# Optimization experiments

Hardware: AMD Instinct MI355X
Metric: run time of the kernel (lower is better)

## Reference

```python
import jax, jax.numpy as jnp
import numpy as np

N = 2048       # num nodes
E = 4096       # num edges
D_NODE = 128
D_EDGE = 128
H = 4          # heads
DH = D_EDGE // H
C = 16         # num classes
NODE_K = N // 2   # node_k_ratio = 0.5
EDGE_K = E // 2   # edge_k_ratio = 0.5
NEG = -1e9


def setup_inputs() -> dict:
    key = jax.random.key(0)
    ks = jax.random.split(key, 16)
    w = lambda k, shape: jax.random.normal(k, shape, jnp.float32) * 0.02
    return {
        "node_features": jax.random.normal(ks[0], (N, D_NODE), jnp.float32),
        "edge_features": jax.random.normal(ks[1], (E, D_EDGE), jnp.float32),
        "edge_index": jax.random.randint(ks[2], (2, E), 0, N, jnp.int32),
        # ImportanceRouter: scalar scores per node / edge
        "w_router_n": w(ks[3], (D_NODE,)),
        "w_router_e": w(ks[4], (D_EDGE,)),
        # EdgeAttention projections
        "w_e": w(ks[5], (D_EDGE, D_EDGE)),
        "w_n": w(ks[6], (D_NODE, D_EDGE)),
        "w_q": w(ks[7], (D_EDGE, D_EDGE)),
        "w_k": w(ks[8], (D_EDGE, D_EDGE)),
        "w_v": w(ks[9], (D_EDGE, D_EDGE)),
        "w_o": w(ks[10], (D_EDGE, D_EDGE)),
        # classifier MLP: Linear -> GELU -> Linear
        "w1": w(ks[11], (D_EDGE, D_EDGE)),
        "b1": jnp.zeros((D_EDGE,), jnp.float32),
        "w2": w(ks[12], (D_EDGE, C)),
        "b2": jnp.zeros((C,), jnp.float32),
    }


def reference(node_features, edge_features, edge_index,
              w_router_n, w_router_e,
              w_e, w_n, w_q, w_k, w_v, w_o,
              w1, b1, w2, b2):
    src, dst = edge_index[0], edge_index[1]

    # --- ImportanceRouter: node/edge scores ---
    ns = node_features @ w_router_n   # [N]
    es = edge_features @ w_router_e   # [E]

    # --- apply_top_k(node_k_ratio=0.5, edge_k_ratio=0.5) ---
    _, nidx = jax.lax.top_k(ns, NODE_K)
    node_mask = jnp.zeros((N,), bool).at[nidx].set(True)
    _, eidx = jax.lax.top_k(es, EDGE_K)
    edge_topk = jnp.zeros((E,), bool).at[eidx].set(True)
    edge_mask = edge_topk & node_mask[src] & node_mask[dst]   # [E]

    ef = edge_features * edge_mask[:, None].astype(edge_features.dtype)

    # --- build_edge_adjacency: edges sharing a node attend to each other ---
    adj = ((src[:, None] == src[None, :]) | (src[:, None] == dst[None, :]) |
           (dst[:, None] == src[None, :]) | (dst[:, None] == dst[None, :]))  # [E,E]

    # --- EdgeAttention: edge rep mixes edge feats and endpoint node feats ---
    h = ef @ w_e + (node_features[src] + node_features[dst]) @ w_n   # [E, D_EDGE]
    q = (h @ w_q).reshape(E, H, DH)
    k = (h @ w_k).reshape(E, H, DH)
    v = (h @ w_v).reshape(E, H, DH)
    scores = jnp.einsum('ehd,fhd->hef', q, k) / np.float32(np.sqrt(DH))  # [H,E,E]
    scores = jnp.where(adj[None, :, :], scores, NEG)
    attn = jax.nn.softmax(scores, axis=-1)
    o = jnp.einsum('hef,fhd->ehd', attn, v).reshape(E, D_EDGE) @ w_o    # [E, D_EDGE]

    # --- classifier: Linear -> GELU -> Linear ---
    x = jax.nn.gelu(o @ w1 + b1)
    logits = x @ w2 + b2            # [E, C]
    return logits
```

## Files before the change

kernel.cpp:

```cpp
#include <hip/hip_runtime.h>
#include <hip/hip_bf16.h>
#include <math.h>

#define NN 2048
#define NE 4096
#define D 128
#define NODE_K 1024
#define EDGE_K 2048
#define CAP 64

typedef const __hip_bfloat16* bfp;
typedef unsigned short u16;
typedef __attribute__((ext_vector_type(8))) short short8;
typedef __attribute__((ext_vector_type(4))) float floatx4;

#define MFMA16(a, b, c) __builtin_amdgcn_mfma_f32_16x16x32_bf16(a, b, c, 0, 0, 0)

__device__ __forceinline__ float b2f(__hip_bfloat16 x) { return __bfloat162float(x); }

__device__ __forceinline__ float ldx(const void* p, size_t i, int f) {
  return f ? ((const float*)p)[i] : b2f(((bfp)p)[i]);
}
__device__ __forceinline__ float4 ldx4(const void* p, size_t i4, int f) {
  if (f) return ((const float4*)p)[i4];
  ushort4 u = ((const ushort4*)p)[i4];
  float4 r;
  r.x = __uint_as_float(((unsigned)u.x) << 16);
  r.y = __uint_as_float(((unsigned)u.y) << 16);
  r.z = __uint_as_float(((unsigned)u.z) << 16);
  r.w = __uint_as_float(((unsigned)u.w) << 16);
  return r;
}

__device__ __forceinline__ void split2(float x, u16& hi, u16& lo) {
  unsigned u = __float_as_uint(x);
  unsigned h = (u + 0x7FFFu + ((u >> 16) & 1u)) >> 16;
  hi = (u16)h;
  float r = x - __uint_as_float(h << 16);
  unsigned v = __float_as_uint(r);
  lo = (u16)((v + 0x7FFFu + ((v >> 16) & 1u)) >> 16);
}
__device__ __forceinline__ void build_frags(const float* v8, short8& fh, short8& fl) {
  #pragma unroll
  for (int i = 0; i < 8; ++i) {
    u16 h, l;
    split2(v8[i], h, l);
    fh[i] = (short)h; fl[i] = (short)l;
  }
}

__device__ __forceinline__ int detect_f(const u16* raw, int* s4) {
  int t = threadIdx.x;
  int weird = 0;
  for (int i = t; i < 1024; i += blockDim.x) {
    unsigned int bits = ((unsigned int)raw[i]) << 16;
    float x = __uint_as_float(bits);
    float ax = fabsf(x);
    if (!(ax <= 1e3f) || (x != 0.f && ax < 1e-12f)) weird++;
  }
  #pragma unroll
  for (int m = 32; m >= 1; m >>= 1) weird += __shfl_xor(weird, m);
  int nw = (int)blockDim.x >> 6;
  if ((t & 63) == 0) s4[t >> 6] = weird;
  __syncthreads();
  int tot = 0;
  for (int i = 0; i < nw; ++i) tot += s4[i];
  return (tot > 50) ? 1 : 0;
}

struct K1Args {
  const void *nf, *ef, *wrn, *wre;
  const void* w[7];
  float *ns, *es;
  int *deg, *flag;
  u16 *wtHi, *wtLo;
  u16 *feHi, *feLo;
};

#define SCORE_BLOCKS ((NN + NE) / 4)
#define WPREP_BLOCKS 112
#define FSPLIT_BLOCKS 192
__global__ __launch_bounds__(256) void scores_prep_kernel(K1Args a) {
  __shared__ int s4[4];
  int b = blockIdx.x, t = threadIdx.x;
  int f = detect_f((const u16*)a.nf, s4);
  if (b < SCORE_BLOCKS) {
    int wid = b * 4 + (t >> 6), lane = t & 63;
    const void* base; const void* w; float* out; size_t r0;
    if (wid < NN) { base = a.nf; r0 = (size_t)wid * D; w = a.wrn; out = a.ns + wid; }
    else { int r = wid - NN; base = a.ef; r0 = (size_t)r * D; w = a.wre; out = a.es + r; }
    double p = (double)ldx(base, r0 + lane, f) * (double)ldx(w, lane, f)
             + (double)ldx(base, r0 + lane + 64, f) * (double)ldx(w, lane + 64, f);
    #pragma unroll
    for (int m = 32; m >= 1; m >>= 1) p += __shfl_xor(p, m);
    if (lane == 0) *out = (float)p;
  } else if (b == SCORE_BLOCKS) {
    if (t == 0) a.flag[0] = f;
    for (int i = t; i < NN; i += 256) a.deg[i] = 0;
  } else if (b <= SCORE_BLOCKS + WPREP_BLOCKS) {
    int tau = (b - SCORE_BLOCKS - 1) * 256 + t;
    int w = tau >> 12, rem = tau & 4095;
    int n = rem >> 5, k0 = (rem & 31) * 4;
    ushort4 hi, lo;
    split2(ldx(a.w[w], (size_t)(k0 + 0) * 128 + n, f), hi.x, lo.x);
    split2(ldx(a.w[w], (size_t)(k0 + 1) * 128 + n, f), hi.y, lo.y);
    split2(ldx(a.w[w], (size_t)(k0 + 2) * 128 + n, f), hi.z, lo.z);
    split2(ldx(a.w[w], (size_t)(k0 + 3) * 128 + n, f), hi.w, lo.w);
    ((ushort4*)a.wtHi)[tau] = hi;
    ((ushort4*)a.wtLo)[tau] = lo;
  } else {
    int fb = b - SCORE_BLOCKS - 1 - WPREP_BLOCKS;
    #pragma unroll
    for (int i = 0; i < 4; ++i) {
      int g4 = fb * 1024 + i * 256 + t;
      float4 x = (g4 < NN * D / 4) ? ldx4(a.nf, g4, f)
                                   : ldx4(a.ef, g4 - NN * D / 4, f);
      ushort4 hi, lo;
      split2(x.x, hi.x, lo.x);
      split2(x.y, hi.y, lo.y);
      split2(x.z, hi.z, lo.z);
      split2(x.w, hi.w, lo.w);
      ((ushort4*)a.feHi)[g4] = hi;
      ((ushort4*)a.feLo)[g4] = lo;
    }
  }
}

#define NMB (NN / 4)
#define EMB (NE / 4)
__global__ __launch_bounds__(256) void mask_lists_kernel(
    const float* __restrict__ ns, const float* __restrict__ es,
    const int* __restrict__ src, const int* __restrict__ dst,
    int* __restrict__ node_mask, int* __restrict__ edge_topk,
    int* __restrict__ deg, int* __restrict__ lists) {
  __shared__ __align__(16) float s[NE];
  int b = blockIdx.x, t = threadIdx.x;
  if (b < NMB) {
    for (int i = t; i < NN / 4; i += 256) ((float4*)s)[i] = ((const float4*)ns)[i];
    __syncthreads();
    int i = b * 4 + (t >> 6), lane = t & 63;
    float si = s[i];
    int rank = 0;
    for (int j = lane; j < NN; j += 64) {
      float sj = s[j];
      rank += (sj > si) || (sj == si && j < i);
    }
    #pragma unroll
    for (int m = 32; m >= 1; m >>= 1) rank += __shfl_xor(rank, m);
    if (lane == 0) node_mask[i] = (rank < NODE_K) ? 1 : 0;
  } else if (b < NMB + EMB) {
    for (int i = t; i < NE / 4; i += 256) ((float4*)s)[i] = ((const float4*)es)[i];
    __syncthreads();
    int i = (b - NMB) * 4 + (t >> 6), lane = t & 63;
    float si = s[i];
    int rank = 0;
    for (int j = lane; j < NE; j += 64) {
      float sj = s[j];
      rank += (sj > si) || (sj == si && j < i);
    }
    #pragma unroll
    for (int m = 32; m >= 1; m >>= 1) rank += __shfl_xor(rank, m);
    if (lane == 0) edge_topk[i] = (rank < EDGE_K) ? 1 : 0;
  } else {
    int e = (b - NMB - EMB) * 256 + t;
    if (e < NE) {
      int sn = src[e], dn = dst[e];
      int p = atomicAdd(&deg[sn], 1);
      if (p >= 0 && p < CAP) lists[sn * CAP + p] = e;
      if (dn != sn) {
        p = atomicAdd(&deg[dn], 1);
        if (p >= 0 && p < CAP) lists[dn * CAP + p] = e;
      }
    }
  }
}

__global__ __launch_bounds__(512) void h_qkv_mfma_kernel(
    const u16* __restrict__ feHi, const u16* __restrict__ feLo,
    const int* __restrict__ src, const int* __restrict__ dst,
    const int* __restrict__ node_mask, const int* __restrict__ edge_topk,
    const u16* __restrict__ wtHi, const u16* __restrict__ wtLo,
    float* __restrict__ qkv) {
  __shared__ __align__(16) float hf[8 * 64 * 4];
  int t = threadIdx.x;
  int wave = t >> 6, lane = t & 63;
  int qd = lane >> 4, c = lane & 15;
  int row0 = blockIdx.x * 16;
  int e = row0 + c;
  int sn = src[e], dn = dst[e];
  bool em = edge_topk[e] && node_mask[sn] && node_mask[dn];
  int n0 = wave * 16;
  const u16* efH = feHi + (size_t)NN * D;
  const u16* efL = feLo + (size_t)NN * D;
  const short8 z8 = {0, 0, 0, 0, 0, 0, 0, 0};

  short8 A1h[4], A1l[4], Sh[4], Sl[4], Dh[4], Dl[4];
  short8 BEh[4], BEl[4], BNh[4], BNl[4];
  #pragma unroll
  for (int ks = 0; ks < 4; ++ks) {
    int k0 = ks * 32 + qd * 8;
    A1h[ks] = *(const short8*)(efH + (size_t)e * D + k0);
    A1l[ks] = *(const short8*)(efL + (size_t)e * D + k0);
    Sh[ks]  = *(const short8*)(feHi + (size_t)sn * D + k0);
    Sl[ks]  = *(const short8*)(feLo + (size_t)sn * D + k0);
    Dh[ks]  = *(const short8*)(feHi + (size_t)dn * D + k0);
    Dl[ks]  = *(const short8*)(feLo + (size_t)dn * D + k0);
    size_t bo = (size_t)(n0 + c) * 128 + k0;
    BEh[ks] = *(const short8*)(wtHi + bo);
    BEl[ks] = *(const short8*)(wtLo + bo);
    BNh[ks] = *(const short8*)(wtHi + 16384 + bo);
    BNl[ks] = *(const short8*)(wtLo + 16384 + bo);
  }
  if (!em) {
    #pragma unroll
    for (int ks = 0; ks < 4; ++ks) { A1h[ks] = z8; A1l[ks] = z8; }
  }
  floatx4 accE = {0.f, 0.f, 0.f, 0.f};
  floatx4 accN = {0.f, 0.f, 0.f, 0.f};
  #pragma unroll
  for (int ks = 0; ks < 4; ++ks) {
    accE = MFMA16(A1h[ks], BEh[ks], accE);
    accN = MFMA16(Sh[ks], BNh[ks], accN);
    accE = MFMA16(A1l[ks], BEh[ks], accE);
    accN = MFMA16(Sl[ks], BNh[ks], accN);
    accE = MFMA16(A1h[ks], BEl[ks], accE);
    accN = MFMA16(Sh[ks], BNl[ks], accN);
    accN = MFMA16(Dh[ks], BNh[ks], accN);
    accN = MFMA16(Dl[ks], BNh[ks], accN);
    accN = MFMA16(Dh[ks], BNl[ks], accN);
  }
  {
    int np = n0 + c;
    int kd = np >> 5, qq = (np >> 3) & 3, half = (c >> 2) & 1, j4 = c & 3;
    #pragma unroll
    for (int r = 0; r < 4; ++r)
      hf[((kd * 2 + half) * 64 + qq * 16 + 4 * qd + r) * 4 + j4] = accE[r] + accN[r];
  }
  short8 BQh[4], BQl[4], BKh[4], BKl[4], BVh[4], BVl[4];
  #pragma unroll
  for (int ks = 0; ks < 4; ++ks) {
    size_t bo = (size_t)(n0 + c) * 128 + ks * 32 + qd * 8;
    BQh[ks] = *(const short8*)(wtHi + 2 * 16384 + bo);
    BQl[ks] = *(const short8*)(wtLo + 2 * 16384 + bo);
    BKh[ks] = *(const short8*)(wtHi + 3 * 16384 + bo);
    BKl[ks] = *(const short8*)(wtLo + 3 * 16384 + bo);
    BVh[ks] = *(const short8*)(wtHi + 4 * 16384 + bo);
    BVl[ks] = *(const short8*)(wtLo + 4 * 16384 + bo);
  }
  __syncthreads();
  floatx4 aq = {0.f, 0.f, 0.f, 0.f};
  floatx4 ak = {0.f, 0.f, 0.f, 0.f};
  floatx4 av = {0.f, 0.f, 0.f, 0.f};
  #pragma unroll
  for (int ks = 0; ks < 4; ++ks) {
    float4 p0 = *(const float4*)&hf[((ks * 2 + 0) * 64 + lane) * 4];
    float4 p1 = *(const float4*)&hf[((ks * 2 + 1) * 64 + lane) * 4];
    float v8[8] = {p0.x, p0.y, p0.z, p0.w, p1.x, p1.y, p1.z, p1.w};
    short8 ah, al;
    build_frags(v8, ah, al);
    aq = MFMA16(ah, BQh[ks], aq);
    ak = MFMA16(ah, BKh[ks], ak);
    av = MFMA16(ah, BVh[ks], av);
    aq = MFMA16(al, BQh[ks], aq);
    ak = MFMA16(al, BKh[ks], ak);
    av = MFMA16(al, BVh[ks], av);
    aq = MFMA16(ah, BQl[ks], aq);
    ak = MFMA16(ah, BKl[ks], ak);
    av = MFMA16(ah, BVl[ks], av);
  }
  #pragma unroll
  for (int r = 0; r < 4; ++r) {
    size_t ro = (size_t)(row0 + 4 * qd + r) * D + n0 + c;
    qkv[ro] = aq[r];
    qkv[(size_t)NE * D + ro] = ak[r];
    qkv[(size_t)2 * NE * D + ro] = av[r];
  }
}

__global__ void attn_kernel(const float* __restrict__ q, const float* __restrict__ k,
                            const float* __restrict__ v, const int* __restrict__ src,
                            const int* __restrict__ dst, const int* __restrict__ deg,
                            const int* __restrict__ lists, float* __restrict__ ao) {
  int e = blockIdx.x;
  int j = threadIdx.x;
  float qj = q[(size_t)e * D + j];
  int sn = src[e], dn = dst[e];
  float m = -1e30f, l = 0.f, acc = 0.f;
  const float scale = 0.17677669529663687f;
  int degA = max(0, min(deg[sn], CAP));
  for (int i = 0; i < degA; ++i) {
    int fe = lists[sn * CAP + i];
    float p = qj * k[(size_t)fe * D + j];
    p += __shfl_xor(p, 16); p += __shfl_xor(p, 8); p += __shfl_xor(p, 4);
    p += __shfl_xor(p, 2);  p += __shfl_xor(p, 1);
    float s = p * scale;
    float vj = v[(size_t)fe * D + j];
    float mn = fmaxf(m, s);
    float corr = expf(m - mn);
    float w = expf(s - mn);
    l = l * corr + w;
    acc = acc * corr + w * vj;
    m = mn;
  }
  if (dn != sn) {
    int degB = max(0, min(deg[dn], CAP));
    for (int i = 0; i < degB; ++i) {
      int fe = lists[dn * CAP + i];
      if (src[fe] == sn || dst[fe] == sn) continue;
      float p = qj * k[(size_t)fe * D + j];
      p += __shfl_xor(p, 16); p += __shfl_xor(p, 8); p += __shfl_xor(p, 4);
      p += __shfl_xor(p, 2);  p += __shfl_xor(p, 1);
      float s = p * scale;
      float vj = v[(size_t)fe * D + j];
      float mn = fmaxf(m, s);
      float corr = expf(m - mn);
      float w = expf(s - mn);
      l = l * corr + w;
      acc = acc * corr + w * vj;
      m = mn;
    }
  }
  ao[(size_t)e * D + j] = acc / fmaxf(l, 1e-37f);
}

__global__ __launch_bounds__(512) void o_mlp_mfma_kernel(
    const float* __restrict__ ao,
    const u16* __restrict__ wtHi, const u16* __restrict__ wtLo,
    const void* __restrict__ b1, const void* __restrict__ w2,
    const void* __restrict__ b2, const int* __restrict__ flag,
    void* __restrict__ out) {
  __shared__ __align__(16) float hf[8 * 64 * 4];
  __shared__ float xl[16 * 132];
  __shared__ float w2l[128 * 16];
  int t = threadIdx.x;
  int wave = t >> 6, lane = t & 63;
  int qd = lane >> 4, c = lane & 15;
  int f = flag[0];
  int row0 = blockIdx.x * 16;
  int n0 = wave * 16;

  short8 BOh[4], BOl[4], B1h[4], B1l[4];
  #pragma unroll
  for (int ks = 0; ks < 4; ++ks) {
    size_t bo = (size_t)(n0 + c) * 128 + ks * 32 + qd * 8;
    BOh[ks] = *(const short8*)(wtHi + 5 * 16384 + bo);
    BOl[ks] = *(const short8*)(wtLo + 5 * 16384 + bo);
    B1h[ks] = *(const short8*)(wtHi + 6 * 16384 + bo);
    B1l[ks] = *(const short8*)(wtLo + 6 * 16384 + bo);
  }
  floatx4 acc = {0.f, 0.f, 0.f, 0.f};
  #pragma unroll
  for (int ks = 0; ks < 4; ++ks) {
    int k0 = ks * 32 + qd * 8;
    const float* ap = ao + (size_t)(row0 + c) * D + k0;
    float4 p0 = *(const float4*)ap;
    float4 p1 = *(const float4*)(ap + 4);
    float v8[8] = {p0.x, p0.y, p0.z, p0.w, p1.x, p1.y, p1.z, p1.w};
    short8 ah, al;
    build_frags(v8, ah, al);
    acc = MFMA16(ah, BOh[ks], acc);
    acc = MFMA16(al, BOh[ks], acc);
    acc = MFMA16(ah, BOl[ks], acc);
  }
  {
    int np = n0 + c;
    int kd = np >> 5, qq = (np >> 3) & 3, half = (c >> 2) & 1, j4 = c & 3;
    #pragma unroll
    for (int r = 0; r < 4; ++r)
      hf[((kd * 2 + half) * 64 + qq * 16 + 4 * qd + r) * 4 + j4] = acc[r];
  }
  __syncthreads();
  floatx4 a2c = {0.f, 0.f, 0.f, 0.f};
  #pragma unroll
  for (int ks = 0; ks < 4; ++ks) {
    float4 p0 = *(const float4*)&hf[((ks * 2 + 0) * 64 + lane) * 4];
    float4 p1 = *(const float4*)&hf[((ks * 2 + 1) * 64 + lane) * 4];
    float v8[8] = {p0.x, p0.y, p0.z, p0.w, p1.x, p1.y, p1.z, p1.w};
    short8 ah, al;
    build_frags(v8, ah, al);
    a2c = MFMA16(ah, B1h[ks], a2c);
    a2c = MFMA16(al, B1h[ks], a2c);
    a2c = MFMA16(ah, B1l[ks], a2c);
  }
  float bj = ldx(b1, n0 + c, f);
  #pragma unroll
  for (int r = 0; r < 4; ++r) {
    float u = a2c[r] + bj;
    float inner = 0.7978845608028654f * (u + 0.044715f * u * u * u);
    xl[(4 * qd + r) * 132 + n0 + c] = 0.5f * u * (1.f + tanhf(inner));
  }
  for (int i = t; i < D * 16; i += 512) w2l[i] = ldx(w2, i, f);
  __syncthreads();
  if (t < 256) {
    int r = t >> 4, cc = t & 15;
    float s = 0.f;
    for (int kk = 0; kk < D; ++kk) s += xl[r * 132 + kk] * w2l[kk * 16 + cc];
    s += ldx(b2, cc, f);
    int idx = (row0 + r) * 16 + cc;
    if (f) ((float*)out)[idx] = s;
    else ((__hip_bfloat16*)out)[idx] = __float2bfloat16(s);
  }
}

extern "C" void kernel_launch(void* const* d_in, const int* in_sizes, int n_in,
                              void* d_out, int out_size, void* d_ws, size_t ws_size,
                              hipStream_t stream) {
  const int* eidx = (const int*)d_in[2];
  const int* src = eidx;
  const int* dst = eidx + NE;

  size_t off = 0;
  char* base = (char*)d_ws;
  auto alloc = [&](size_t nbytes) -> void* {
    void* p = base + off;
    off += (nbytes + 255) & ~(size_t)255;
    return p;
  };
  int* flag      = (int*)alloc(256);
  float* ns      = (float*)alloc(NN * sizeof(float));
  float* es      = (float*)alloc(NE * sizeof(float));
  int* node_mask = (int*)alloc(NN * sizeof(int));
  int* edge_topk = (int*)alloc(NE * sizeof(int));
  int* deg       = (int*)alloc(NN * sizeof(int));
  int* lists     = (int*)alloc((size_t)NN * CAP * sizeof(int));
  u16* wtHi      = (u16*)alloc((size_t)7 * 16384 * sizeof(u16));
  u16* wtLo      = (u16*)alloc((size_t)7 * 16384 * sizeof(u16));
  u16* feHi      = (u16*)alloc((size_t)(NN + NE) * D * sizeof(u16));
  u16* feLo      = (u16*)alloc((size_t)(NN + NE) * D * sizeof(u16));
  float* qkv     = (float*)alloc((size_t)3 * NE * D * sizeof(float));
  float* ao      = (float*)alloc((size_t)NE * D * sizeof(float));
  float* qb = qkv, *kb = qkv + NE * D, *vb = qkv + 2 * NE * D;

  K1Args a1;
  a1.nf = d_in[0]; a1.ef = d_in[1]; a1.wrn = d_in[3]; a1.wre = d_in[4];
  a1.w[0] = d_in[5];  a1.w[1] = d_in[6];  a1.w[2] = d_in[7];
  a1.w[3] = d_in[8];  a1.w[4] = d_in[9];  a1.w[5] = d_in[10]; a1.w[6] = d_in[11];
  a1.ns = ns; a1.es = es; a1.deg = deg; a1.flag = flag;
  a1.wtHi = wtHi; a1.wtLo = wtLo; a1.feHi = feHi; a1.feLo = feLo;

  scores_prep_kernel<<<SCORE_BLOCKS + 1 + WPREP_BLOCKS + FSPLIT_BLOCKS, 256, 0,
                       stream>>>(a1);
  mask_lists_kernel<<<NMB + EMB + NE / 256, 256, 0, stream>>>(
      ns, es, src, dst, node_mask, edge_topk, deg, lists);
  h_qkv_mfma_kernel<<<NE / 16, 512, 0, stream>>>(
      feHi, feLo, src, dst, node_mask, edge_topk, wtHi, wtLo, qkv);
  attn_kernel<<<NE, 128, 0, stream>>>(qb, kb, vb, src, dst, deg, lists, ao);
  o_mlp_mfma_kernel<<<NE / 16, 512, 0, stream>>>(
      ao, wtHi, wtLo, d_in[12], d_in[13], d_in[14], flag, d_out);
}
```

Baseline: 139.2 us.

## Split attention neighbor loop across four thread groups and vectorize top-k and MLP loops

The attention kernel now runs 512 threads per edge, with four groups each handling every fourth neighbor. The partial online-softmax states (max, sum, accumulator) are merged through shared memory at the end, which shortens the serial neighbor chain per edge. The top-k ranking reads scores directly from global memory as float4 instead of first staging them in shared memory, and the final 128x16 classifier stage stores w2 transposed so its dot product can use float4 reads. The split attention adds a block barrier and extra exp calls for the merge, and most groups sit idle when node degree is small.

```diff
diff --git a/kernel.cpp b/kernel.cpp
--- a/kernel.cpp
+++ b/kernel.cpp
@@ -133,30 +133,33 @@
     const int* __restrict__ src, const int* __restrict__ dst,
     int* __restrict__ node_mask, int* __restrict__ edge_topk,
     int* __restrict__ deg, int* __restrict__ lists) {
-  __shared__ __align__(16) float s[NE];
   int b = blockIdx.x, t = threadIdx.x;
   if (b < NMB) {
-    for (int i = t; i < NN / 4; i += 256) ((float4*)s)[i] = ((const float4*)ns)[i];
-    __syncthreads();
     int i = b * 4 + (t >> 6), lane = t & 63;
-    float si = s[i];
+    float si = ns[i];
     int rank = 0;
-    for (int j = lane; j < NN; j += 64) {
-      float sj = s[j];
-      rank += (sj > si) || (sj == si && j < i);
+    for (int j4 = lane; j4 < NN / 4; j4 += 64) {
+      float4 sj = ((const float4*)ns)[j4];
+      int j = j4 * 4;
+      rank += (sj.x > si) || (sj.x == si && j + 0 < i);
+      rank += (sj.y > si) || (sj.y == si && j + 1 < i);
+      rank += (sj.z > si) || (sj.z == si && j + 2 < i);
+      rank += (sj.w > si) || (sj.w == si && j + 3 < i);
     }
     #pragma unroll
     for (int m = 32; m >= 1; m >>= 1) rank += __shfl_xor(rank, m);
     if (lane == 0) node_mask[i] = (rank < NODE_K) ? 1 : 0;
   } else if (b < NMB + EMB) {
-    for (int i = t; i < NE / 4; i += 256) ((float4*)s)[i] = ((const float4*)es)[i];
-    __syncthreads();
     int i = (b - NMB) * 4 + (t >> 6), lane = t & 63;
-    float si = s[i];
+    float si = es[i];
     int rank = 0;
-    for (int j = lane; j < NE; j += 64) {
-      float sj = s[j];
-      rank += (sj > si) || (sj == si && j < i);
+    for (int j4 = lane; j4 < NE / 4; j4 += 64) {
+      float4 sj = ((const float4*)es)[j4];
+      int j = j4 * 4;
+      rank += (sj.x > si) || (sj.x == si && j + 0 < i);
+      rank += (sj.y > si) || (sj.y == si && j + 1 < i);
+      rank += (sj.z > si) || (sj.z == si && j + 2 < i);
+      rank += (sj.w > si) || (sj.w == si && j + 3 < i);
     }
     #pragma unroll
     for (int m = 32; m >= 1; m >>= 1) rank += __shfl_xor(rank, m);
@@ -277,24 +280,27 @@
   }
 }
 
-__global__ void attn_kernel(const float* __restrict__ q, const float* __restrict__ k,
-                            const float* __restrict__ v, const int* __restrict__ src,
-                            const int* __restrict__ dst, const int* __restrict__ deg,
-                            const int* __restrict__ lists, float* __restrict__ ao) {
+__global__ __launch_bounds__(512) void attn_kernel(
+    const float* __restrict__ q, const float* __restrict__ k,
+    const float* __restrict__ v, const int* __restrict__ src,
+    const int* __restrict__ dst, const int* __restrict__ deg,
+    const int* __restrict__ lists, float* __restrict__ ao) {
+  __shared__ float sm[4][128], sl[4][128], sa[4][128];
   int e = blockIdx.x;
-  int j = threadIdx.x;
-  float qj = q[(size_t)e * D + j];
+  int t = threadIdx.x;
+  int par = t >> 7, jj = t & 127;
+  float qj = q[(size_t)e * D + jj];
   int sn = src[e], dn = dst[e];
   float m = -1e30f, l = 0.f, acc = 0.f;
   const float scale = 0.17677669529663687f;
   int degA = max(0, min(deg[sn], CAP));
-  for (int i = 0; i < degA; ++i) {
+  for (int i = par; i < degA; i += 4) {
     int fe = lists[sn * CAP + i];
-    float p = qj * k[(size_t)fe * D + j];
+    float p = qj * k[(size_t)fe * D + jj];
     p += __shfl_xor(p, 16); p += __shfl_xor(p, 8); p += __shfl_xor(p, 4);
     p += __shfl_xor(p, 2);  p += __shfl_xor(p, 1);
     float s = p * scale;
-    float vj = v[(size_t)fe * D + j];
+    float vj = v[(size_t)fe * D + jj];
     float mn = fmaxf(m, s);
     float corr = expf(m - mn);
     float w = expf(s - mn);
@@ -304,14 +310,14 @@
   }
   if (dn != sn) {
     int degB = max(0, min(deg[dn], CAP));
-    for (int i = 0; i < degB; ++i) {
+    for (int i = par; i < degB; i += 4) {
       int fe = lists[dn * CAP + i];
       if (src[fe] == sn || dst[fe] == sn) continue;
-      float p = qj * k[(size_t)fe * D + j];
+      float p = qj * k[(size_t)fe * D + jj];
       p += __shfl_xor(p, 16); p += __shfl_xor(p, 8); p += __shfl_xor(p, 4);
       p += __shfl_xor(p, 2);  p += __shfl_xor(p, 1);
       float s = p * scale;
-      float vj = v[(size_t)fe * D + j];
+      float vj = v[(size_t)fe * D + jj];
       float mn = fmaxf(m, s);
       float corr = expf(m - mn);
       float w = expf(s - mn);
@@ -320,7 +326,22 @@
       m = mn;
     }
   }
-  ao[(size_t)e * D + j] = acc / fmaxf(l, 1e-37f);
+  sm[par][jj] = m; sl[par][jj] = l; sa[par][jj] = acc;
+  __syncthreads();
+  if (par == 0) {
+    float M = m;
+    #pragma unroll
+    for (int p2 = 1; p2 < 4; ++p2) M = fmaxf(M, sm[p2][jj]);
+    float cs = expf(m - M);
+    float L = l * cs, A = acc * cs;
+    #pragma unroll
+    for (int p2 = 1; p2 < 4; ++p2) {
+      float c2 = expf(sm[p2][jj] - M);
+      L += sl[p2][jj] * c2;
+      A += sa[p2][jj] * c2;
+    }
+    ao[(size_t)e * D + jj] = A / fmaxf(L, 1e-37f);
+  }
 }
 
 __global__ __launch_bounds__(512) void o_mlp_mfma_kernel(
@@ -330,8 +351,8 @@
     const void* __restrict__ b2, const int* __restrict__ flag,
     void* __restrict__ out) {
   __shared__ __align__(16) float hf[8 * 64 * 4];
-  __shared__ float xl[16 * 132];
-  __shared__ float w2l[128 * 16];
+  __shared__ __align__(16) float xl[16 * 132];
+  __shared__ __align__(16) float w2t[16 * 132];
   int t = threadIdx.x;
   int wave = t >> 6, lane = t & 63;
   int qd = lane >> 4, c = lane & 15;
@@ -389,12 +410,21 @@
     float inner = 0.7978845608028654f * (u + 0.044715f * u * u * u);
     xl[(4 * qd + r) * 132 + n0 + c] = 0.5f * u * (1.f + tanhf(inner));
   }
-  for (int i = t; i < D * 16; i += 512) w2l[i] = ldx(w2, i, f);
+  for (int i = t; i < D * 16; i += 512) {
+    int kk = i >> 4, cc = i & 15;
+    w2t[cc * 132 + kk] = ldx(w2, i, f);
+  }
   __syncthreads();
   if (t < 256) {
     int r = t >> 4, cc = t & 15;
+    const float4* xr = (const float4*)&xl[r * 132];
+    const float4* wr = (const float4*)&w2t[cc * 132];
     float s = 0.f;
-    for (int kk = 0; kk < D; ++kk) s += xl[r * 132 + kk] * w2l[kk * 16 + cc];
+    #pragma unroll
+    for (int k4 = 0; k4 < D / 4; ++k4) {
+      float4 xa = xr[k4], wb = wr[k4];
+      s += xa.x * wb.x + xa.y * wb.y + xa.z * wb.z + xa.w * wb.w;
+    }
     s += ldx(b2, cc, f);
     int idx = (row0 + r) * 16 + cc;
     if (f) ((float*)out)[idx] = s;
@@ -444,7 +474,7 @@
       ns, es, src, dst, node_mask, edge_topk, deg, lists);
   h_qkv_mfma_kernel<<<NE / 16, 512, 0, stream>>>(
       feHi, feLo, src, dst, node_mask, edge_topk, wtHi, wtLo, qkv);
-  attn_kernel<<<NE, 128, 0, stream>>>(qb, kb, vb, src, dst, deg, lists, ao);
+  attn_kernel<<<NE, 512, 0, stream>>>(qb, kb, vb, src, dst, deg, lists, ao);
   o_mlp_mfma_kernel<<<NE / 16, 512, 0, stream>>>(
       ao, wtHi, wtLo, d_in[12], d_in[13], d_in[14], flag, d_out);
 }
```

After: 144.9 us. 1.04x slower.

## Fuse top-k masking into QKV kernel and attention into MLP kernel

Applied to the files above, without the earlier changes.

Five launches become three. The adjacency-list build moves into the prep kernel as a single block using LDS atomics. The top-k rank computation moves into the QKV kernel, computed only for the edges and endpoints each block needs. Attention is fused with the output projection and MLP in a 1024-thread block, so the attention output stays in LDS, and the w2 dot product is vectorised through a transposed LDS copy. This removes launch overhead and the global round trip for ao and the masks. The cost is a serial one-block list build, recomputation of node ranks per edge, and __syncthreads calls placed inside divergent branches, which is fragile.

```diff
diff --git a/kernel.cpp b/kernel.cpp
--- a/kernel.cpp
+++ b/kernel.cpp
@@ -49,10 +49,11 @@
   }
 }
 
-__device__ __forceinline__ int detect_f(const u16* raw, int* s4) {
+template <int NT>
+__device__ __forceinline__ int detect_f(const u16* raw, int* s8) {
   int t = threadIdx.x;
   int weird = 0;
-  for (int i = t; i < 1024; i += blockDim.x) {
+  for (int i = t; i < 1024; i += NT) {
     unsigned int bits = ((unsigned int)raw[i]) << 16;
     float x = __uint_as_float(bits);
     float ax = fabsf(x);
@@ -60,19 +61,20 @@
   }
   #pragma unroll
   for (int m = 32; m >= 1; m >>= 1) weird += __shfl_xor(weird, m);
-  int nw = (int)blockDim.x >> 6;
-  if ((t & 63) == 0) s4[t >> 6] = weird;
+  if ((t & 63) == 0) s8[t >> 6] = weird;
   __syncthreads();
   int tot = 0;
-  for (int i = 0; i < nw; ++i) tot += s4[i];
+  #pragma unroll
+  for (int i = 0; i < NT / 64; ++i) tot += s8[i];
   return (tot > 50) ? 1 : 0;
 }
 
 struct K1Args {
   const void *nf, *ef, *wrn, *wre;
   const void* w[7];
+  const int *src, *dst;
   float *ns, *es;
-  int *deg, *flag;
+  int *deg, *lists, *flag;
   u16 *wtHi, *wtLo;
   u16 *feHi, *feLo;
 };
@@ -80,10 +82,11 @@
 #define SCORE_BLOCKS ((NN + NE) / 4)
 #define WPREP_BLOCKS 112
 #define FSPLIT_BLOCKS 192
-__global__ __launch_bounds__(256) void scores_prep_kernel(K1Args a) {
-  __shared__ int s4[4];
+#define K1_BLOCKS (SCORE_BLOCKS + WPREP_BLOCKS + FSPLIT_BLOCKS + 1)
+__global__ __launch_bounds__(256) void scores_prep_lists_kernel(K1Args a) {
+  __shared__ int s8[4];
   int b = blockIdx.x, t = threadIdx.x;
-  int f = detect_f((const u16*)a.nf, s4);
+  int f = detect_f<256>((const u16*)a.nf, s8);
   if (b < SCORE_BLOCKS) {
     int wid = b * 4 + (t >> 6), lane = t & 63;
     const void* base; const void* w; float* out; size_t r0;
@@ -94,11 +97,8 @@
     #pragma unroll
     for (int m = 32; m >= 1; m >>= 1) p += __shfl_xor(p, m);
     if (lane == 0) *out = (float)p;
-  } else if (b == SCORE_BLOCKS) {
-    if (t == 0) a.flag[0] = f;
-    for (int i = t; i < NN; i += 256) a.deg[i] = 0;
-  } else if (b <= SCORE_BLOCKS + WPREP_BLOCKS) {
-    int tau = (b - SCORE_BLOCKS - 1) * 256 + t;
+  } else if (b < SCORE_BLOCKS + WPREP_BLOCKS) {
+    int tau = (b - SCORE_BLOCKS) * 256 + t;
     int w = tau >> 12, rem = tau & 4095;
     int n = rem >> 5, k0 = (rem & 31) * 4;
     ushort4 hi, lo;
@@ -108,8 +108,8 @@
     split2(ldx(a.w[w], (size_t)(k0 + 3) * 128 + n, f), hi.w, lo.w);
     ((ushort4*)a.wtHi)[tau] = hi;
     ((ushort4*)a.wtLo)[tau] = lo;
-  } else {
-    int fb = b - SCORE_BLOCKS - 1 - WPREP_BLOCKS;
+  } else if (b < SCORE_BLOCKS + WPREP_BLOCKS + FSPLIT_BLOCKS) {
+    int fb = b - SCORE_BLOCKS - WPREP_BLOCKS;
     #pragma unroll
     for (int i = 0; i < 4; ++i) {
       int g4 = fb * 1024 + i * 256 + t;
@@ -123,72 +123,65 @@
       ((ushort4*)a.feHi)[g4] = hi;
       ((ushort4*)a.feLo)[g4] = lo;
     }
-  }
-}
-
-#define NMB (NN / 4)
-#define EMB (NE / 4)
-__global__ __launch_bounds__(256) void mask_lists_kernel(
+  } else {
+    __shared__ int ldeg[NN];
+    for (int i = t; i < NN; i += 256) ldeg[i] = 0;
+    __syncthreads();
+    #pragma unroll
+    for (int i = 0; i < NE / 256; ++i) {
+      int e = i * 256 + t;
+      int sn = a.src[e], dn = a.dst[e];
+      int p = atomicAdd(&ldeg[sn], 1);
+      if (p < CAP) a.lists[sn * CAP + p] = e;
+      if (dn != sn) {
+        p = atomicAdd(&ldeg[dn], 1);
+        if (p < CAP) a.lists[dn * CAP + p] = e;
+      }
+    }
+    __syncthreads();
+    for (int i = t; i < NN; i += 256) a.deg[i] = ldeg[i];
+    if (t == 0) a.flag[0] = f;
+  }
+}
+
+__global__ __launch_bounds__(512) void h_qkv_mfma_kernel(
     const float* __restrict__ ns, const float* __restrict__ es,
-    const int* __restrict__ src, const int* __restrict__ dst,
-    int* __restrict__ node_mask, int* __restrict__ edge_topk,
-    int* __restrict__ deg, int* __restrict__ lists) {
-  __shared__ __align__(16) float s[NE];
-  int b = blockIdx.x, t = threadIdx.x;
-  if (b < NMB) {
-    for (int i = t; i < NN / 4; i += 256) ((float4*)s)[i] = ((const float4*)ns)[i];
-    __syncthreads();
-    int i = b * 4 + (t >> 6), lane = t & 63;
-    float si = s[i];
-    int rank = 0;
-    for (int j = lane; j < NN; j += 64) {
-      float sj = s[j];
-      rank += (sj > si) || (sj == si && j < i);
-    }
-    #pragma unroll
-    for (int m = 32; m >= 1; m >>= 1) rank += __shfl_xor(rank, m);
-    if (lane == 0) node_mask[i] = (rank < NODE_K) ? 1 : 0;
-  } else if (b < NMB + EMB) {
-    for (int i = t; i < NE / 4; i += 256) ((float4*)s)[i] = ((const float4*)es)[i];
-    __syncthreads();
-    int i = (b - NMB) * 4 + (t >> 6), lane = t & 63;
-    float si = s[i];
-    int rank = 0;
-    for (int j = lane; j < NE; j += 64) {
-      float sj = s[j];
-      rank += (sj > si) || (sj == si && j < i);
-    }
-    #pragma unroll
-    for (int m = 32; m >= 1; m >>= 1) rank += __shfl_xor(rank, m);
-    if (lane == 0) edge_topk[i] = (rank < EDGE_K) ? 1 : 0;
-  } else {
-    int e = (b - NMB - EMB) * 256 + t;
-    if (e < NE) {
-      int sn = src[e], dn = dst[e];
-      int p = atomicAdd(&deg[sn], 1);
-      if (p >= 0 && p < CAP) lists[sn * CAP + p] = e;
-      if (dn != sn) {
-        p = atomicAdd(&deg[dn], 1);
-        if (p >= 0 && p < CAP) lists[dn * CAP + p] = e;
-      }
-    }
-  }
-}
-
-__global__ __launch_bounds__(512) void h_qkv_mfma_kernel(
     const u16* __restrict__ feHi, const u16* __restrict__ feLo,
     const int* __restrict__ src, const int* __restrict__ dst,
-    const int* __restrict__ node_mask, const int* __restrict__ edge_topk,
     const u16* __restrict__ wtHi, const u16* __restrict__ wtLo,
     float* __restrict__ qkv) {
   __shared__ __align__(16) float hf[8 * 64 * 4];
+  __shared__ int s_msk[3][16];
   int t = threadIdx.x;
   int wave = t >> 6, lane = t & 63;
   int qd = lane >> 4, c = lane & 15;
   int row0 = blockIdx.x * 16;
+
+  for (int task = wave; task < 48; task += 8) {
+    int kind = task >> 4, ti = task & 15;
+    int e2 = row0 + ti;
+    const float* arr; int len, K, tgt;
+    if (kind == 0) { arr = es; len = NE; K = EDGE_K; tgt = e2; }
+    else { arr = ns; len = NN; K = NODE_K; tgt = (kind == 1) ? src[e2] : dst[e2]; }
+    float si = arr[tgt];
+    int rank = 0;
+    for (int j4 = lane; j4 < (len >> 2); j4 += 64) {
+      float4 sj = ((const float4*)arr)[j4];
+      int j = j4 * 4;
+      rank += (sj.x > si) || (sj.x == si && j + 0 < tgt);
+      rank += (sj.y > si) || (sj.y == si && j + 1 < tgt);
+      rank += (sj.z > si) || (sj.z == si && j + 2 < tgt);
+      rank += (sj.w > si) || (sj.w == si && j + 3 < tgt);
+    }
+    #pragma unroll
+    for (int m = 32; m >= 1; m >>= 1) rank += __shfl_xor(rank, m);
+    if (lane == 0) s_msk[kind][ti] = (rank < K) ? 1 : 0;
+  }
+  __syncthreads();
+
   int e = row0 + c;
   int sn = src[e], dn = dst[e];
-  bool em = edge_topk[e] && node_mask[sn] && node_mask[dn];
+  bool em = s_msk[0][c] && s_msk[1][c] && s_msk[2][c];
   int n0 = wave * 16;
   const u16* efH = feHi + (size_t)NN * D;
   const u16* efL = feLo + (size_t)NN * D;
@@ -277,124 +270,151 @@
   }
 }
 
-__global__ void attn_kernel(const float* __restrict__ q, const float* __restrict__ k,
-                            const float* __restrict__ v, const int* __restrict__ src,
-                            const int* __restrict__ dst, const int* __restrict__ deg,
-                            const int* __restrict__ lists, float* __restrict__ ao) {
-  int e = blockIdx.x;
-  int j = threadIdx.x;
-  float qj = q[(size_t)e * D + j];
-  int sn = src[e], dn = dst[e];
-  float m = -1e30f, l = 0.f, acc = 0.f;
-  const float scale = 0.17677669529663687f;
-  int degA = max(0, min(deg[sn], CAP));
-  for (int i = 0; i < degA; ++i) {
-    int fe = lists[sn * CAP + i];
-    float p = qj * k[(size_t)fe * D + j];
-    p += __shfl_xor(p, 16); p += __shfl_xor(p, 8); p += __shfl_xor(p, 4);
-    p += __shfl_xor(p, 2);  p += __shfl_xor(p, 1);
-    float s = p * scale;
-    float vj = v[(size_t)fe * D + j];
-    float mn = fmaxf(m, s);
-    float corr = expf(m - mn);
-    float w = expf(s - mn);
-    l = l * corr + w;
-    acc = acc * corr + w * vj;
-    m = mn;
-  }
-  if (dn != sn) {
-    int degB = max(0, min(deg[dn], CAP));
-    for (int i = 0; i < degB; ++i) {
-      int fe = lists[dn * CAP + i];
-      if (src[fe] == sn || dst[fe] == sn) continue;
-      float p = qj * k[(size_t)fe * D + j];
-      p += __shfl_xor(p, 16); p += __shfl_xor(p, 8); p += __shfl_xor(p, 4);
-      p += __shfl_xor(p, 2);  p += __shfl_xor(p, 1);
-      float s = p * scale;
-      float vj = v[(size_t)fe * D + j];
-      float mn = fmaxf(m, s);
-      float corr = expf(m - mn);
-      float w = expf(s - mn);
-      l = l * corr + w;
-      acc = acc * corr + w * vj;
-      m = mn;
-    }
-  }
-  ao[(size_t)e * D + j] = acc / fmaxf(l, 1e-37f);
-}
-
-__global__ __launch_bounds__(512) void o_mlp_mfma_kernel(
-    const float* __restrict__ ao,
+__global__ __launch_bounds__(1024) void attn_mlp_kernel(
+    const float* __restrict__ qkv, const int* __restrict__ src,
+    const int* __restrict__ dst, const int* __restrict__ deg,
+    const int* __restrict__ lists,
     const u16* __restrict__ wtHi, const u16* __restrict__ wtLo,
     const void* __restrict__ b1, const void* __restrict__ w2,
     const void* __restrict__ b2, const int* __restrict__ flag,
     void* __restrict__ out) {
+  __shared__ __align__(16) float ao_lds[16 * 132];
   __shared__ __align__(16) float hf[8 * 64 * 4];
-  __shared__ float xl[16 * 132];
-  __shared__ float w2l[128 * 16];
+  __shared__ __align__(16) float xl[16 * 132];
+  __shared__ __align__(16) float w2t[16 * 132];
   int t = threadIdx.x;
   int wave = t >> 6, lane = t & 63;
+  int row0 = blockIdx.x * 16;
+
+  {
+    const float* qb = qkv;
+    const float* kb = qkv + (size_t)NE * D;
+    const float* vb = qkv + (size_t)2 * NE * D;
+    int half = lane >> 5, l5 = lane & 31;
+    int d0 = l5 + 64 * half;
+    int d1 = d0 + 32;
+    int e = row0 + wave;
+    int sn = src[e], dn = dst[e];
+    const float scale = 0.17677669529663687f;
+    float q0 = qb[(size_t)e * D + d0], q1 = qb[(size_t)e * D + d1];
+    float m0 = -1e30f, l0 = 0.f, a0 = 0.f;
+    float m1 = -1e30f, l1 = 0.f, a1 = 0.f;
+    int degA = max(0, min(deg[sn], CAP));
+    for (int i = 0; i < degA; ++i) {
+      int fe = lists[sn * CAP + i];
+      float p0 = q0 * kb[(size_t)fe * D + d0];
+      float p1 = q1 * kb[(size_t)fe * D + d1];
+      #pragma unroll
+      for (int mk = 16; mk >= 1; mk >>= 1) {
+        p0 += __shfl_xor(p0, mk);
+        p1 += __shfl_xor(p1, mk);
+      }
+      float v0 = vb[(size_t)fe * D + d0], v1 = vb[(size_t)fe * D + d1];
+      float s0 = p0 * scale, s1 = p1 * scale;
+      float n0_ = fmaxf(m0, s0), n1_ = fmaxf(m1, s1);
+      float c0 = expf(m0 - n0_), c1 = expf(m1 - n1_);
+      float w0 = expf(s0 - n0_), w1 = expf(s1 - n1_);
+      l0 = l0 * c0 + w0; a0 = a0 * c0 + w0 * v0; m0 = n0_;
+      l1 = l1 * c1 + w1; a1 = a1 * c1 + w1 * v1; m1 = n1_;
+    }
+    if (dn != sn) {
+      int degB = max(0, min(deg[dn], CAP));
+      for (int i = 0; i < degB; ++i) {
+        int fe = lists[dn * CAP + i];
+        if (src[fe] == sn || dst[fe] == sn) continue;
+        float p0 = q0 * kb[(size_t)fe * D + d0];
+        float p1 = q1 * kb[(size_t)fe * D + d1];
+        #pragma unroll
+        for (int mk = 16; mk >= 1; mk >>= 1) {
+          p0 += __shfl_xor(p0, mk);
+          p1 += __shfl_xor(p1, mk);
+        }
+        float v0 = vb[(size_t)fe * D + d0], v1 = vb[(size_t)fe * D + d1];
+        float s0 = p0 * scale, s1 = p1 * scale;
+        float n0_ = fmaxf(m0, s0), n1_ = fmaxf(m1, s1);
+        float c0 = expf(m0 - n0_), c1 = expf(m1 - n1_);
+        float w0 = expf(s0 - n0_), w1 = expf(s1 - n1_);
+        l0 = l0 * c0 + w0; a0 = a0 * c0 + w0 * v0; m0 = n0_;
+        l1 = l1 * c1 + w1; a1 = a1 * c1 + w1 * v1; m1 = n1_;
+      }
+    }
+    ao_lds[wave * 132 + d0] = a0 / fmaxf(l0, 1e-37f);
+    ao_lds[wave * 132 + d1] = a1 / fmaxf(l1, 1e-37f);
+  }
+  __syncthreads();
+
+  int f = flag[0];
   int qd = lane >> 4, c = lane & 15;
-  int f = flag[0];
-  int row0 = blockIdx.x * 16;
   int n0 = wave * 16;
-
-  short8 BOh[4], BOl[4], B1h[4], B1l[4];
-  #pragma unroll
-  for (int ks = 0; ks < 4; ++ks) {
-    size_t bo = (size_t)(n0 + c) * 128 + ks * 32 + qd * 8;
-    BOh[ks] = *(const short8*)(wtHi + 5 * 16384 + bo);
-    BOl[ks] = *(const short8*)(wtLo + 5 * 16384 + bo);
-    B1h[ks] = *(const short8*)(wtHi + 6 * 16384 + bo);
-    B1l[ks] = *(const short8*)(wtLo + 6 * 16384 + bo);
-  }
-  floatx4 acc = {0.f, 0.f, 0.f, 0.f};
-  #pragma unroll
-  for (int ks = 0; ks < 4; ++ks) {
-    int k0 = ks * 32 + qd * 8;
-    const float* ap = ao + (size_t)(row0 + c) * D + k0;
-    float4 p0 = *(const float4*)ap;
-    float4 p1 = *(const float4*)(ap + 4);
-    float v8[8] = {p0.x, p0.y, p0.z, p0.w, p1.x, p1.y, p1.z, p1.w};
-    short8 ah, al;
-    build_frags(v8, ah, al);
-    acc = MFMA16(ah, BOh[ks], acc);
-    acc = MFMA16(al, BOh[ks], acc);
-    acc = MFMA16(ah, BOl[ks], acc);
-  }
-  {
-    int np = n0 + c;
-    int kd = np >> 5, qq = (np >> 3) & 3, half = (c >> 2) & 1, j4 = c & 3;
-    #pragma unroll
-    for (int r = 0; r < 4; ++r)
-      hf[((kd * 2 + half) * 64 + qq * 16 + 4 * qd + r) * 4 + j4] = acc[r];
-  }
-  __syncthreads();
-  floatx4 a2c = {0.f, 0.f, 0.f, 0.f};
-  #pragma unroll
-  for (int ks = 0; ks < 4; ++ks) {
-    float4 p0 = *(const float4*)&hf[((ks * 2 + 0) * 64 + lane) * 4];
-    float4 p1 = *(const float4*)&hf[((ks * 2 + 1) * 64 + lane) * 4];
-    float v8[8] = {p0.x, p0.y, p0.z, p0.w, p1.x, p1.y, p1.z, p1.w};
-    short8 ah, al;
-    build_frags(v8, ah, al);
-    a2c = MFMA16(ah, B1h[ks], a2c);
-    a2c = MFMA16(al, B1h[ks], a2c);
-    a2c = MFMA16(ah, B1l[ks], a2c);
-  }
-  float bj = ldx(b1, n0 + c, f);
-  #pragma unroll
-  for (int r = 0; r < 4; ++r) {
-    float u = a2c[r] + bj;
-    float inner = 0.7978845608028654f * (u + 0.044715f * u * u * u);
-    xl[(4 * qd + r) * 132 + n0 + c] = 0.5f * u * (1.f + tanhf(inner));
-  }
-  for (int i = t; i < D * 16; i += 512) w2l[i] = ldx(w2, i, f);
+  if (t < 512) {
+    short8 BOh[4], BOl[4], B1h[4], B1l[4];
+    #pragma unroll
+    for (int ks = 0; ks < 4; ++ks) {
+      size_t bo = (size_t)(n0 + c) * 128 + ks * 32 + qd * 8;
+      BOh[ks] = *(const short8*)(wtHi + 5 * 16384 + bo);
+      BOl[ks] = *(const short8*)(wtLo + 5 * 16384 + bo);
+      B1h[ks] = *(const short8*)(wtHi + 6 * 16384 + bo);
+      B1l[ks] = *(const short8*)(wtLo + 6 * 16384 + bo);
+    }
+    floatx4 acc = {0.f, 0.f, 0.f, 0.f};
+    #pragma unroll
+    for (int ks = 0; ks < 4; ++ks) {
+      int k0 = ks * 32 + qd * 8;
+      const float* ap = &ao_lds[c * 132 + k0];
+      float4 p0 = *(const float4*)ap;
+      float4 p1 = *(const float4*)(ap + 4);
+      float v8[8] = {p0.x, p0.y, p0.z, p0.w, p1.x, p1.y, p1.z, p1.w};
+      short8 ah, al;
+      build_frags(v8, ah, al);
+      acc = MFMA16(ah, BOh[ks], acc);
+      acc = MFMA16(al, BOh[ks], acc);
+      acc = MFMA16(ah, BOl[ks], acc);
+    }
+    {
+      int np = n0 + c;
+      int kd = np >> 5, qq = (np >> 3) & 3, half = (c >> 2) & 1, j4 = c & 3;
+      #pragma unroll
+      for (int r = 0; r < 4; ++r)
+        hf[((kd * 2 + half) * 64 + qq * 16 + 4 * qd + r) * 4 + j4] = acc[r];
+    }
+    __syncthreads();
+    floatx4 a2c = {0.f, 0.f, 0.f, 0.f};
+    #pragma unroll
+    for (int ks = 0; ks < 4; ++ks) {
+      float4 p0 = *(const float4*)&hf[((ks * 2 + 0) * 64 + lane) * 4];
+      float4 p1 = *(const float4*)&hf[((ks * 2 + 1) * 64 + lane) * 4];
+      float v8[8] = {p0.x, p0.y, p0.z, p0.w, p1.x, p1.y, p1.z, p1.w};
+      short8 ah, al;
+      build_frags(v8, ah, al);
+      a2c = MFMA16(ah, B1h[ks], a2c);
+      a2c = MFMA16(al, B1h[ks], a2c);
+      a2c = MFMA16(ah, B1l[ks], a2c);
+    }
+    float bj = ldx(b1, n0 + c, f);
+    #pragma unroll
+    for (int r = 0; r < 4; ++r) {
+      float u = a2c[r] + bj;
+      float inner = 0.7978845608028654f * (u + 0.044715f * u * u * u);
+      xl[(4 * qd + r) * 132 + n0 + c] = 0.5f * u * (1.f + tanhf(inner));
+    }
+  } else {
+    for (int i = t - 512; i < D * 16; i += 512) {
+      int kk = i >> 4, cc = i & 15;
+      w2t[cc * 132 + kk] = ldx(w2, i, f);
+    }
+    __syncthreads();
+  }
   __syncthreads();
   if (t < 256) {
     int r = t >> 4, cc = t & 15;
+    const float4* xr = (const float4*)&xl[r * 132];
+    const float4* wr = (const float4*)&w2t[cc * 132];
     float s = 0.f;
-    for (int kk = 0; kk < D; ++kk) s += xl[r * 132 + kk] * w2l[kk * 16 + cc];
+    #pragma unroll
+    for (int k4 = 0; k4 < D / 4; ++k4) {
+      float4 xa = xr[k4], wb = wr[k4];
+      s += xa.x * wb.x + xa.y * wb.y + xa.z * wb.z + xa.w * wb.w;
+    }
     s += ldx(b2, cc, f);
     int idx = (row0 + r) * 16 + cc;
     if (f) ((float*)out)[idx] = s;
@@ -419,8 +439,6 @@
   int* flag      = (int*)alloc(256);
   float* ns      = (float*)alloc(NN * sizeof(float));
   float* es      = (float*)alloc(NE * sizeof(float));
-  int* node_mask = (int*)alloc(NN * sizeof(int));
-  int* edge_topk = (int*)alloc(NE * sizeof(int));
   int* deg       = (int*)alloc(NN * sizeof(int));
   int* lists     = (int*)alloc((size_t)NN * CAP * sizeof(int));
   u16* wtHi      = (u16*)alloc((size_t)7 * 16384 * sizeof(u16));
@@ -428,23 +446,21 @@
   u16* feHi      = (u16*)alloc((size_t)(NN + NE) * D * sizeof(u16));
   u16* feLo      = (u16*)alloc((size_t)(NN + NE) * D * sizeof(u16));
   float* qkv     = (float*)alloc((size_t)3 * NE * D * sizeof(float));
-  float* ao      = (float*)alloc((size_t)NE * D * sizeof(float));
   float* qb = qkv, *kb = qkv + NE * D, *vb = qkv + 2 * NE * D;
+  (void)qb; (void)kb; (void)vb;
 
   K1Args a1;
   a1.nf = d_in[0]; a1.ef = d_in[1]; a1.wrn = d_in[3]; a1.wre = d_in[4];
   a1.w[0] = d_in[5];  a1.w[1] = d_in[6];  a1.w[2] = d_in[7];
   a1.w[3] = d_in[8];  a1.w[4] = d_in[9];  a1.w[5] = d_in[10]; a1.w[6] = d_in[11];
-  a1.ns = ns; a1.es = es; a1.deg = deg; a1.flag = flag;
+  a1.src = src; a1.dst = dst;
+  a1.ns = ns; a1.es = es; a1.deg = deg; a1.lists = lists; a1.flag = flag;
   a1.wtHi = wtHi; a1.wtLo = wtLo; a1.feHi = feHi; a1.feLo = feLo;
 
-  scores_prep_kernel<<<SCORE_BLOCKS + 1 + WPREP_BLOCKS + FSPLIT_BLOCKS, 256, 0,
-                       stream>>>(a1);
-  mask_lists_kernel<<<NMB + EMB + NE / 256, 256, 0, stream>>>(
-      ns, es, src, dst, node_mask, edge_topk, deg, lists);
+  scores_prep_lists_kernel<<<K1_BLOCKS, 256, 0, stream>>>(a1);
   h_qkv_mfma_kernel<<<NE / 16, 512, 0, stream>>>(
-      feHi, feLo, src, dst, node_mask, edge_topk, wtHi, wtLo, qkv);
-  attn_kernel<<<NE, 128, 0, stream>>>(qb, kb, vb, src, dst, deg, lists, ao);
-  o_mlp_mfma_kernel<<<NE / 16, 512, 0, stream>>>(
-      ao, wtHi, wtLo, d_in[12], d_in[13], d_in[14], flag, d_out);
-}
+      ns, es, feHi, feLo, src, dst, wtHi, wtLo, qkv);
+  attn_mlp_kernel<<<NE / 16, 1024, 0, stream>>>(
+      qkv, src, dst, deg, lists, wtHi, wtLo,
+      d_in[12], d_in[13], d_in[14], flag, d_out);
+}
```

New measurement: 161.0 us. +15.7%, slower.
